# Optimization experiments

Hardware: AMD Instinct MI355X
Metric: run time of the kernel (lower is better)

Reference implementation:

```python
import jax, jax.numpy as jnp
import numpy as np

B, L, T, D, H, DH = 8, 1024, 1024, 768, 12, 64
SPATIAL_DIM = 5


def setup_inputs() -> dict:
    key = jax.random.key(0)
    ks = jax.random.split(key, 12)
    scale = 1.0 / np.sqrt(D)
    inp = {
        "q": jax.random.normal(ks[0], (B, L, D), dtype=jnp.float32),
        "k": jax.random.normal(ks[1], (B, T, D), dtype=jnp.float32),
        "v": jax.random.normal(ks[2], (B, T, D), dtype=jnp.float32),
        "pairwise_locs": jax.random.normal(ks[3], (B, L, T, SPATIAL_DIM), dtype=jnp.float32),
        # last 64 key positions are padding in every batch row (never all-True)
        "key_padding_mask": jnp.broadcast_to(jnp.arange(T) >= T - 64, (B, T)),
        "Wq": jax.random.normal(ks[4], (D, H * DH), dtype=jnp.float32) * scale,
        "bq": jnp.zeros((H * DH,), dtype=jnp.float32),
        "Wk": jax.random.normal(ks[5], (D, H * DH), dtype=jnp.float32) * scale,
        "bk": jnp.zeros((H * DH,), dtype=jnp.float32),
        "Wv": jax.random.normal(ks[6], (D, H * DH), dtype=jnp.float32) * scale,
        "bv": jnp.zeros((H * DH,), dtype=jnp.float32),
        "Wo": jax.random.normal(ks[7], (H * DH, D), dtype=jnp.float32) * scale,
        "bo": jnp.zeros((D,), dtype=jnp.float32),
    }
    return inp


def reference(q, k, v, pairwise_locs, key_padding_mask, Wq, bq, Wk, bk, Wv, bv, Wo, bo):
    # pairwise_locs is accepted but unused in this forward path (as in the source).
    b, l, _ = q.shape
    t = k.shape[1]
    qh = (q @ Wq + bq).reshape(b, l, H, DH)  # b l h d
    kh = (k @ Wk + bk).reshape(b, t, H, DH)  # b t h d
    vh = (v @ Wv + bv).reshape(b, t, H, DH)  # b t h d
    attn = jnp.einsum('blhd,bthd->bhlt', qh, kh) / jnp.sqrt(jnp.float32(DH))
    attn = jnp.where(key_padding_mask[:, None, None, :], -jnp.inf, attn)
    fused_attn = jax.nn.softmax(attn, axis=-1)
    out = jnp.einsum('bhlt,bthd->blhd', fused_attn, vh).reshape(b, l, H * DH)
    return out @ Wo + bo  # dropout is identity in eval mode
```

## Files before the change

### kernel.cpp

```cpp
#include <hip/hip_runtime.h>
#include <hip/hip_bf16.h>
#include <cstdint>
#include <cstddef>
#include <cmath>

#define NB 8
#define NL 1024
#define NT 1024
#define ND 768
#define NH 12
#define NDH 64
#define NM (NB*NL)

typedef short short8 __attribute__((ext_vector_type(8)));
typedef unsigned short ushort4v __attribute__((ext_vector_type(4)));
typedef unsigned int uint4v __attribute__((ext_vector_type(4)));
typedef float f32x4 __attribute__((ext_vector_type(4)));
typedef float float4v __attribute__((ext_vector_type(4)));

__device__ __forceinline__ unsigned short f2bf(float f) {
  union { __hip_bfloat16 h; unsigned short u; } cv;
  cv.h = __float2bfloat16(f);
  return cv.u;
}
__device__ __forceinline__ unsigned pk2(float lo, float hi) {
  return (unsigned)f2bf(lo) | ((unsigned)f2bf(hi) << 16);
}
__device__ __forceinline__ short8 cvt8(float4v x0, float4v x1) {
  union { short8 s; uint4v u; } r;
  r.u = (uint4v){pk2(x0[0], x0[1]), pk2(x0[2], x0[3]),
                 pk2(x1[0], x1[1]), pk2(x1[2], x1[3])};
  return r.s;
}
__device__ __forceinline__ void gll16(const void* g, void* l) {
  __builtin_amdgcn_global_load_lds(
      (const __attribute__((address_space(1))) unsigned int*)g,
      (__attribute__((address_space(3))) unsigned int*)l, 16, 0, 0);
}

__global__ __launch_bounds__(256) void wt_kernel(
    const float* __restrict__ W0, const float* __restrict__ W1,
    const float* __restrict__ W2, const float* __restrict__ W3,
    unsigned short* __restrict__ Wt) {
  __shared__ float tile[32][33];
  const float* W = blockIdx.z == 0 ? W0 : blockIdx.z == 1 ? W1 : blockIdx.z == 2 ? W2 : W3;
  const int k0 = blockIdx.x * 32, n0 = blockIdx.y * 32;
  const int tx = threadIdx.x & 31, ty = threadIdx.x >> 5;
  for (int r = ty; r < 32; r += 8) tile[r][tx] = W[(size_t)(k0 + r) * ND + n0 + tx];
  __syncthreads();
  unsigned short* out = Wt + (size_t)blockIdx.z * ND * ND;
  for (int r = ty; r < 32; r += 8) out[(size_t)(n0 + r) * ND + k0 + tx] = f2bf(tile[tx][r]);
}

template<int MODE>
__global__ __launch_bounds__(256) void gemm_kernel(
    const float* __restrict__ Af0, const float* __restrict__ Af1,
    const unsigned short* __restrict__ Ab, const unsigned short* __restrict__ Wt,
    const float* __restrict__ bias0, const float* __restrict__ bias1,
    unsigned short* __restrict__ outb0, unsigned short* __restrict__ outb1,
    float* __restrict__ outf) {
  constexpr bool AF32 = (MODE != 3);
  __shared__ __align__(16) unsigned char AsRaw[AF32 ? 128 * 64 * 4 : 128 * 64 * 2];
  __shared__ __align__(16) unsigned short Bs[128 * 64];
  const int tid = threadIdx.x, lane = tid & 63, w = tid >> 6;
  const int c = lane & 15, g = lane >> 4;
  const int wrow = w & 1, wcol = w >> 1;
  const int l8 = lane >> 3, l7 = lane & 7, csw = l7 ^ l8;
  const int mbase = blockIdx.x * 128, nbase = blockIdx.y * 128;
  const int z = (MODE == 0) ? blockIdx.z : MODE;

  const float* Af = AF32 ? ((MODE == 0 && z == 1) ? Af1 : Af0) : nullptr;
  const unsigned short* Bt = Wt + (size_t)z * ND * ND;
  const float* bias = (MODE == 0 && z == 1) ? bias1 : bias0;

  f32x4 acc[4][4];
#pragma unroll
  for (int m = 0; m < 4; m++)
#pragma unroll
    for (int n = 0; n < 4; n++) acc[m][n] = (f32x4){0.f, 0.f, 0.f, 0.f};

  for (int k0 = 0; k0 < ND; k0 += 64) {
    if (AF32) {
      float* Asf = (float*)AsRaw;
#pragma unroll
      for (int it = 0; it < 8; it++) {
        int r0 = it * 16 + w * 4;
        int r = r0 + (lane >> 4);
        int gc = (lane & 15) ^ (r & 15);
        gll16(&Af[(size_t)(mbase + r) * ND + k0 + gc * 4], &Asf[r0 * 64]);
      }
    } else {
      unsigned short* Asb = (unsigned short*)AsRaw;
#pragma unroll
      for (int it = 0; it < 4; it++) {
        int r = it * 32 + w * 8 + l8;
        gll16(&Ab[(size_t)(mbase + r) * ND + k0 + csw * 8], &Asb[(it * 32 + w * 8) * 64]);
      }
    }
#pragma unroll
    for (int it = 0; it < 4; it++) {
      int r = it * 32 + w * 8 + l8;
      gll16(&Bt[(size_t)(nbase + r) * ND + k0 + csw * 8], &Bs[(it * 32 + w * 8) * 64]);
    }
    __syncthreads();

#pragma unroll
    for (int ks = 0; ks < 2; ks++) {
      short8 a[4], b[4];
#pragma unroll
      for (int m = 0; m < 4; m++) {
        int r = wrow * 64 + m * 16 + c;
        if (AF32) {
          const float* Asf = (const float*)AsRaw;
          int cc = ks * 8 + g * 2;
          float4v x0 = *(const float4v*)&Asf[r * 64 + ((cc ^ (r & 15)) * 4)];
          float4v x1 = *(const float4v*)&Asf[r * 64 + (((cc + 1) ^ (r & 15)) * 4)];
          a[m] = cvt8(x0, x1);
        } else {
          const unsigned short* Asb = (const unsigned short*)AsRaw;
          a[m] = *(const short8*)&Asb[r * 64 + (((ks * 4 + g) ^ (c & 7)) * 8)];
        }
      }
#pragma unroll
      for (int n = 0; n < 4; n++) {
        int r = wcol * 64 + n * 16 + c;
        b[n] = *(const short8*)&Bs[r * 64 + (((ks * 4 + g) ^ (c & 7)) * 8)];
      }
#pragma unroll
      for (int m = 0; m < 4; m++)
#pragma unroll
        for (int n = 0; n < 4; n++) {
          if (MODE == 2)
            acc[m][n] = __builtin_amdgcn_mfma_f32_16x16x32_bf16(a[m], b[n], acc[m][n], 0, 0, 0);
          else
            acc[m][n] = __builtin_amdgcn_mfma_f32_16x16x32_bf16(b[n], a[m], acc[m][n], 0, 0, 0);
        }
    }
    __syncthreads();
  }

  if (MODE == 2) {
#pragma unroll
    for (int n = 0; n < 4; n++) {
      const int col = nbase + wcol * 64 + n * 16 + c;
      const float bv = bias[col];
      const int h = col >> 6, dd = col & 63;
#pragma unroll
      for (int m = 0; m < 4; m++) {
        const int r0 = mbase + wrow * 64 + m * 16 + g * 4;
        const int bb = r0 >> 10, t = r0 & (NT - 1);
        ushort4v y;
#pragma unroll
        for (int j = 0; j < 4; j++) y[j] = f2bf(acc[m][n][j] + bv);
        *(ushort4v*)&outb0[((size_t)(bb * NH + h) * NDH + dd) * NT + t] = y;
      }
    }
  } else {
    const float scale = (MODE == 0 && z == 0) ? 0.125f * 1.44269504f : 1.0f;
    unsigned short* outb = (MODE == 0) ? (z == 0 ? outb0 : outb1) : nullptr;
#pragma unroll
    for (int n = 0; n < 4; n++) {
      const int colb = nbase + wcol * 64 + n * 16 + g * 4;
      float4v bv4 = *(const float4v*)&bias[colb];
#pragma unroll
      for (int m = 0; m < 4; m++) {
        const int row = mbase + wrow * 64 + m * 16 + c;
        if (MODE == 3) {
          float4v y;
#pragma unroll
          for (int j = 0; j < 4; j++) y[j] = acc[m][n][j] + bv4[j];
          *(float4v*)&outf[(size_t)row * ND + colb] = y;
        } else {
          ushort4v y;
#pragma unroll
          for (int j = 0; j < 4; j++) y[j] = f2bf((acc[m][n][j] + bv4[j]) * scale);
          *(ushort4v*)&outb[(size_t)row * ND + colb] = y;
        }
      }
    }
  }
}

__global__ __launch_bounds__(256) void attn_kernel(
    const unsigned short* __restrict__ qh, const unsigned short* __restrict__ kh,
    const unsigned short* __restrict__ vhT, const unsigned int* __restrict__ mask,
    unsigned short* __restrict__ ao) {
  __shared__ __align__(16) unsigned short Ks[2][64 * 64];
  __shared__ __align__(16) unsigned short Vs[2][64 * 64];
  __shared__ __align__(16) unsigned short Ps[4][32][72];
  const int tid = threadIdx.x, lane = tid & 63, w = tid >> 6;
  const int c = lane & 15, g = lane >> 4;
  const int l8 = lane >> 3, l7 = lane & 7, csw = l7 ^ l8;
  const int qb = blockIdx.x * 128;
  const int b = blockIdx.y / NH, h = blockIdx.y % NH;
  const size_t kbase = (size_t)b * NT * ND + h * NDH;
  const size_t vbase = (size_t)(b * NH + h) * NDH * NT;

  short8 aq[2][2];
#pragma unroll
  for (int half = 0; half < 2; half++) {
    size_t qrow = (size_t)(b * NL + qb + w * 32 + half * 16 + c) * ND + h * NDH;
#pragma unroll
    for (int ks = 0; ks < 2; ks++)
      aq[half][ks] = *(const short8*)&qh[qrow + ks * 32 + g * 8];
  }

  f32x4 o[2][4];
#pragma unroll
  for (int half = 0; half < 2; half++)
#pragma unroll
    for (int f = 0; f < 4; f++) o[half][f] = (f32x4){0.f, 0.f, 0.f, 0.f};
  float mr[2] = {-1e30f, -1e30f}, lr[2] = {0.f, 0.f};

#pragma unroll
  for (int it = 0; it < 2; it++) {
    int r = w * 16 + it * 8 + l8;
    gll16(&kh[kbase + (size_t)r * ND + csw * 8], &Ks[0][(w * 16 + it * 8) * 64]);
    gll16(&vhT[vbase + (size_t)r * NT + csw * 8], &Vs[0][(w * 16 + it * 8) * 64]);
  }
  __syncthreads();

  for (int t0 = 0; t0 < NT; t0 += 64) {
    const int cur = (t0 >> 6) & 1;
    if (t0 + 64 < NT) {
#pragma unroll
      for (int it = 0; it < 2; it++) {
        int r = w * 16 + it * 8 + l8;
        gll16(&kh[kbase + (size_t)(t0 + 64 + r) * ND + csw * 8],
              &Ks[cur ^ 1][(w * 16 + it * 8) * 64]);
        gll16(&vhT[vbase + (size_t)r * NT + (t0 + 64) + csw * 8],
              &Vs[cur ^ 1][(w * 16 + it * 8) * 64]);
      }
    }

    f32x4 s[2][4];
#pragma unroll
    for (int half = 0; half < 2; half++)
#pragma unroll
      for (int n = 0; n < 4; n++) s[half][n] = (f32x4){0.f, 0.f, 0.f, 0.f};
    __builtin_amdgcn_s_setprio(1);
#pragma unroll
    for (int ks = 0; ks < 2; ks++)
#pragma unroll
      for (int n = 0; n < 4; n++) {
        short8 ak = *(const short8*)&Ks[cur][(n * 16 + c) * 64 + (((ks * 4 + g) ^ (c & 7)) * 8)];
        s[0][n] = __builtin_amdgcn_mfma_f32_16x16x32_bf16(ak, aq[0][ks], s[0][n], 0, 0, 0);
        s[1][n] = __builtin_amdgcn_mfma_f32_16x16x32_bf16(ak, aq[1][ks], s[1][n], 0, 0, 0);
      }
    __builtin_amdgcn_s_setprio(0);

    {
      uint4v mm[4];
      unsigned any = 0;
#pragma unroll
      for (int n = 0; n < 4; n++) {
        mm[n] = *(const uint4v*)&mask[(size_t)b * NT + t0 + n * 16 + g * 4];
        any |= mm[n][0] | mm[n][1] | mm[n][2] | mm[n][3];
      }
      if (__any(any != 0u)) {
#pragma unroll
        for (int n = 0; n < 4; n++)
#pragma unroll
          for (int j = 0; j < 4; j++)
            if (mm[n][j]) { s[0][n][j] = -INFINITY; s[1][n][j] = -INFINITY; }
      }
    }

#pragma unroll
    for (int half = 0; half < 2; half++) {
      float m01 = fmaxf(fmaxf(s[half][0][0], s[half][0][1]), fmaxf(s[half][0][2], s[half][0][3]));
      float m23 = fmaxf(fmaxf(s[half][1][0], s[half][1][1]), fmaxf(s[half][1][2], s[half][1][3]));
      float m45 = fmaxf(fmaxf(s[half][2][0], s[half][2][1]), fmaxf(s[half][2][2], s[half][2][3]));
      float m67 = fmaxf(fmaxf(s[half][3][0], s[half][3][1]), fmaxf(s[half][3][2], s[half][3][3]));
      float mt = fmaxf(fmaxf(m01, m23), fmaxf(m45, m67));
      mt = fmaxf(mt, __shfl_xor(mt, 16, 64));
      mt = fmaxf(mt, __shfl_xor(mt, 32, 64));
      if (!__all(mt <= mr[half] + 8.f)) {
        float mnew = fmaxf(mr[half], mt);
        float alpha = exp2f(mr[half] - mnew);
        lr[half] *= alpha;
#pragma unroll
        for (int f = 0; f < 4; f++)
#pragma unroll
          for (int j = 0; j < 4; j++) o[half][f][j] *= alpha;
        mr[half] = mnew;
      }
      float rs = 0.f;
#pragma unroll
      for (int n = 0; n < 4; n++)
#pragma unroll
        for (int j = 0; j < 4; j++) {
          float p = exp2f(s[half][n][j] - mr[half]);
          s[half][n][j] = p;
          rs += p;
        }
      rs += __shfl_xor(rs, 16, 64);
      rs += __shfl_xor(rs, 32, 64);
      lr[half] += rs;
      unsigned* pr = (unsigned*)&Ps[w][half * 16 + c][0];
#pragma unroll
      for (int n = 0; n < 4; n++) {
        pr[n * 8 + g * 2]     = pk2(s[half][n][0], s[half][n][1]);
        pr[n * 8 + g * 2 + 1] = pk2(s[half][n][2], s[half][n][3]);
      }
    }

    __builtin_amdgcn_s_setprio(1);
#pragma unroll
    for (int ks = 0; ks < 2; ks++) {
      short8 bp0 = *(const short8*)&Ps[w][c][ks * 32 + g * 8];
      short8 bp1 = *(const short8*)&Ps[w][16 + c][ks * 32 + g * 8];
#pragma unroll
      for (int f = 0; f < 4; f++) {
        short8 av = *(const short8*)&Vs[cur][(f * 16 + c) * 64 + (((ks * 4 + g) ^ (c & 7)) * 8)];
        o[0][f] = __builtin_amdgcn_mfma_f32_16x16x32_bf16(av, bp0, o[0][f], 0, 0, 0);
        o[1][f] = __builtin_amdgcn_mfma_f32_16x16x32_bf16(av, bp1, o[1][f], 0, 0, 0);
      }
    }
    __builtin_amdgcn_s_setprio(0);
    __syncthreads();
  }

#pragma unroll
  for (int half = 0; half < 2; half++) {
    float inv = 1.f / lr[half];
    size_t row = (size_t)(b * NL + qb + w * 32 + half * 16 + c) * ND + h * NDH;
#pragma unroll
    for (int f = 0; f < 4; f++) {
      ushort4v y;
#pragma unroll
      for (int j = 0; j < 4; j++) y[j] = f2bf(o[half][f][j] * inv);
      *(ushort4v*)&ao[row + f * 16 + g * 4] = y;
    }
  }
}

extern "C" void kernel_launch(void* const* d_in, const int* in_sizes, int n_in,
                              void* d_out, int out_size, void* d_ws, size_t ws_size,
                              hipStream_t stream) {
  const float* q  = (const float*)d_in[0];
  const float* k  = (const float*)d_in[1];
  const float* v  = (const float*)d_in[2];
  const unsigned int* mask = (const unsigned int*)d_in[4];
  const float* Wq = (const float*)d_in[5];
  const float* bq = (const float*)d_in[6];
  const float* Wk = (const float*)d_in[7];
  const float* bk = (const float*)d_in[8];
  const float* Wv = (const float*)d_in[9];
  const float* bv = (const float*)d_in[10];
  const float* Wo = (const float*)d_in[11];
  const float* bo = (const float*)d_in[12];
  float* out = (float*)d_out;

  unsigned short* ws  = (unsigned short*)d_ws;
  unsigned short* Wt  = ws;
  unsigned short* qhb = Wt + (size_t)4 * ND * ND;
  unsigned short* khb = qhb + (size_t)NM * ND;
  unsigned short* vhT = khb + (size_t)NM * ND;
  unsigned short* aob = vhT + (size_t)NM * ND;

  wt_kernel<<<dim3(ND / 32, ND / 32, 4), 256, 0, stream>>>(Wq, Wk, Wv, Wo, Wt);

  gemm_kernel<0><<<dim3(NM / 128, ND / 128, 2), 256, 0, stream>>>(
      q, k, nullptr, Wt, bq, bk, qhb, khb, nullptr);
  gemm_kernel<2><<<dim3(NM / 128, ND / 128), 256, 0, stream>>>(
      v, nullptr, nullptr, Wt, bv, nullptr, vhT, nullptr, nullptr);

  attn_kernel<<<dim3(NL / 128, NB * NH), 256, 0, stream>>>(qhb, khb, vhT, mask, aob);

  gemm_kernel<3><<<dim3(NM / 128, ND / 128), 256, 0, stream>>>(
      nullptr, nullptr, aob, Wt, bo, nullptr, nullptr, nullptr, out);
}
```

Baseline: 172.6 us.

## Skip fully masked key tiles, defer row-sum reduction, convert A to bf16 on load

The attention loop builds a per-tile ballot of the key padding mask and skips all QK, softmax and PV work for tiles that are entirely masked. The per-row sum is kept as a lane-local vector and reduced across lanes only once at the end, and the max-rescale check is merged for both halves so the cross-lane max runs only when rescaling is needed. The fp32 GEMM A-operand is now loaded through registers and converted to bf16 once before being stored to LDS, replacing the async fp32 LDS staging. This halves the LDS footprint and avoids reconverting per k-step, but it gives up the async global-to-LDS copy.

Result: faster. 168.5 us (-2.4%).

```diff
diff --git a/kernel.cpp b/kernel.cpp
--- a/kernel.cpp
+++ b/kernel.cpp
@@ -15,6 +15,7 @@
 typedef short short8 __attribute__((ext_vector_type(8)));
 typedef unsigned short ushort4v __attribute__((ext_vector_type(4)));
 typedef unsigned int uint4v __attribute__((ext_vector_type(4)));
+typedef unsigned int uint2v __attribute__((ext_vector_type(2)));
 typedef float f32x4 __attribute__((ext_vector_type(4)));
 typedef float float4v __attribute__((ext_vector_type(4)));
 
@@ -26,11 +27,11 @@
 __device__ __forceinline__ unsigned pk2(float lo, float hi) {
   return (unsigned)f2bf(lo) | ((unsigned)f2bf(hi) << 16);
 }
-__device__ __forceinline__ short8 cvt8(float4v x0, float4v x1) {
-  union { short8 s; uint4v u; } r;
-  r.u = (uint4v){pk2(x0[0], x0[1]), pk2(x0[2], x0[3]),
-                 pk2(x1[0], x1[1]), pk2(x1[2], x1[3])};
-  return r.s;
+__device__ __forceinline__ f32x4 vmax4(f32x4 a, f32x4 b) {
+  f32x4 r;
+  r[0] = fmaxf(a[0], b[0]); r[1] = fmaxf(a[1], b[1]);
+  r[2] = fmaxf(a[2], b[2]); r[3] = fmaxf(a[3], b[3]);
+  return r;
 }
 __device__ __forceinline__ void gll16(const void* g, void* l) {
   __builtin_amdgcn_global_load_lds(
@@ -59,8 +60,7 @@
     const float* __restrict__ bias0, const float* __restrict__ bias1,
     unsigned short* __restrict__ outb0, unsigned short* __restrict__ outb1,
     float* __restrict__ outf) {
-  constexpr bool AF32 = (MODE != 3);
-  __shared__ __align__(16) unsigned char AsRaw[AF32 ? 128 * 64 * 4 : 128 * 64 * 2];
+  __shared__ __align__(16) unsigned short As[128 * 64];
   __shared__ __align__(16) unsigned short Bs[128 * 64];
   const int tid = threadIdx.x, lane = tid & 63, w = tid >> 6;
   const int c = lane & 15, g = lane >> 4;
@@ -69,7 +69,7 @@
   const int mbase = blockIdx.x * 128, nbase = blockIdx.y * 128;
   const int z = (MODE == 0) ? blockIdx.z : MODE;
 
-  const float* Af = AF32 ? ((MODE == 0 && z == 1) ? Af1 : Af0) : nullptr;
+  const float* Af = (MODE == 0) ? (z == 0 ? Af0 : Af1) : Af0;
   const unsigned short* Bt = Wt + (size_t)z * ND * ND;
   const float* bias = (MODE == 0 && z == 1) ? bias1 : bias0;
 
@@ -80,21 +80,23 @@
     for (int n = 0; n < 4; n++) acc[m][n] = (f32x4){0.f, 0.f, 0.f, 0.f};
 
   for (int k0 = 0; k0 < ND; k0 += 64) {
-    if (AF32) {
-      float* Asf = (float*)AsRaw;
-#pragma unroll
-      for (int it = 0; it < 8; it++) {
-        int r0 = it * 16 + w * 4;
-        int r = r0 + (lane >> 4);
-        int gc = (lane & 15) ^ (r & 15);
-        gll16(&Af[(size_t)(mbase + r) * ND + k0 + gc * 4], &Asf[r0 * 64]);
+    if (MODE != 3) {
+#pragma unroll
+      for (int i = 0; i < 4; i++) {
+        int id = i * 256 + tid;
+        int r = id >> 3, cc = id & 7;
+        const float* src = &Af[(size_t)(mbase + r) * ND + k0 + cc * 8];
+        float4v x0 = *(const float4v*)src;
+        float4v x1 = *(const float4v*)(src + 4);
+        uint4v y = {pk2(x0[0], x0[1]), pk2(x0[2], x0[3]),
+                    pk2(x1[0], x1[1]), pk2(x1[2], x1[3])};
+        *(uint4v*)&As[r * 64 + ((cc ^ (r & 7)) * 8)] = y;
       }
     } else {
-      unsigned short* Asb = (unsigned short*)AsRaw;
 #pragma unroll
       for (int it = 0; it < 4; it++) {
         int r = it * 32 + w * 8 + l8;
-        gll16(&Ab[(size_t)(mbase + r) * ND + k0 + csw * 8], &Asb[(it * 32 + w * 8) * 64]);
+        gll16(&Ab[(size_t)(mbase + r) * ND + k0 + csw * 8], &As[(it * 32 + w * 8) * 64]);
       }
     }
 #pragma unroll
@@ -110,16 +112,7 @@
 #pragma unroll
       for (int m = 0; m < 4; m++) {
         int r = wrow * 64 + m * 16 + c;
-        if (AF32) {
-          const float* Asf = (const float*)AsRaw;
-          int cc = ks * 8 + g * 2;
-          float4v x0 = *(const float4v*)&Asf[r * 64 + ((cc ^ (r & 15)) * 4)];
-          float4v x1 = *(const float4v*)&Asf[r * 64 + (((cc + 1) ^ (r & 15)) * 4)];
-          a[m] = cvt8(x0, x1);
-        } else {
-          const unsigned short* Asb = (const unsigned short*)AsRaw;
-          a[m] = *(const short8*)&Asb[r * 64 + (((ks * 4 + g) ^ (c & 7)) * 8)];
-        }
+        a[m] = *(const short8*)&As[r * 64 + (((ks * 4 + g) ^ (c & 7)) * 8)];
       }
 #pragma unroll
       for (int n = 0; n < 4; n++) {
@@ -205,12 +198,14 @@
       aq[half][ks] = *(const short8*)&qh[qrow + ks * 32 + g * 8];
   }
 
-  f32x4 o[2][4];
-#pragma unroll
-  for (int half = 0; half < 2; half++)
+  f32x4 o[2][4], lrv[2];
+#pragma unroll
+  for (int half = 0; half < 2; half++) {
+    lrv[half] = (f32x4){0.f, 0.f, 0.f, 0.f};
 #pragma unroll
     for (int f = 0; f < 4; f++) o[half][f] = (f32x4){0.f, 0.f, 0.f, 0.f};
-  float mr[2] = {-1e30f, -1e30f}, lr[2] = {0.f, 0.f};
+  }
+  float mr[2] = {-1e30f, -1e30f};
 
 #pragma unroll
   for (int it = 0; it < 2; it++) {
@@ -233,97 +228,98 @@
       }
     }
 
-    f32x4 s[2][4];
-#pragma unroll
-    for (int half = 0; half < 2; half++)
-#pragma unroll
-      for (int n = 0; n < 4; n++) s[half][n] = (f32x4){0.f, 0.f, 0.f, 0.f};
-    __builtin_amdgcn_s_setprio(1);
-#pragma unroll
-    for (int ks = 0; ks < 2; ks++)
-#pragma unroll
-      for (int n = 0; n < 4; n++) {
-        short8 ak = *(const short8*)&Ks[cur][(n * 16 + c) * 64 + (((ks * 4 + g) ^ (c & 7)) * 8)];
-        s[0][n] = __builtin_amdgcn_mfma_f32_16x16x32_bf16(ak, aq[0][ks], s[0][n], 0, 0, 0);
-        s[1][n] = __builtin_amdgcn_mfma_f32_16x16x32_bf16(ak, aq[1][ks], s[1][n], 0, 0, 0);
-      }
-    __builtin_amdgcn_s_setprio(0);
-
-    {
-      uint4v mm[4];
-      unsigned any = 0;
-#pragma unroll
-      for (int n = 0; n < 4; n++) {
-        mm[n] = *(const uint4v*)&mask[(size_t)b * NT + t0 + n * 16 + g * 4];
-        any |= mm[n][0] | mm[n][1] | mm[n][2] | mm[n][3];
-      }
-      if (__any(any != 0u)) {
+    unsigned long long tm = __ballot(mask[(size_t)b * NT + t0 + lane] != 0u);
+
+    if (tm != ~0ull) {
+      f32x4 s[2][4];
+#pragma unroll
+      for (int half = 0; half < 2; half++)
+#pragma unroll
+        for (int n = 0; n < 4; n++) s[half][n] = (f32x4){0.f, 0.f, 0.f, 0.f};
+      __builtin_amdgcn_s_setprio(1);
+#pragma unroll
+      for (int ks = 0; ks < 2; ks++)
+#pragma unroll
+        for (int n = 0; n < 4; n++) {
+          short8 ak = *(const short8*)&Ks[cur][(n * 16 + c) * 64 + (((ks * 4 + g) ^ (c & 7)) * 8)];
+          s[0][n] = __builtin_amdgcn_mfma_f32_16x16x32_bf16(ak, aq[0][ks], s[0][n], 0, 0, 0);
+          s[1][n] = __builtin_amdgcn_mfma_f32_16x16x32_bf16(ak, aq[1][ks], s[1][n], 0, 0, 0);
+        }
+      __builtin_amdgcn_s_setprio(0);
+
+      if (tm) {
+        unsigned long long tms = tm >> (g * 4);
 #pragma unroll
         for (int n = 0; n < 4; n++)
 #pragma unroll
           for (int j = 0; j < 4; j++)
-            if (mm[n][j]) { s[0][n][j] = -INFINITY; s[1][n][j] = -INFINITY; }
-      }
-    }
-
-#pragma unroll
-    for (int half = 0; half < 2; half++) {
-      float m01 = fmaxf(fmaxf(s[half][0][0], s[half][0][1]), fmaxf(s[half][0][2], s[half][0][3]));
-      float m23 = fmaxf(fmaxf(s[half][1][0], s[half][1][1]), fmaxf(s[half][1][2], s[half][1][3]));
-      float m45 = fmaxf(fmaxf(s[half][2][0], s[half][2][1]), fmaxf(s[half][2][2], s[half][2][3]));
-      float m67 = fmaxf(fmaxf(s[half][3][0], s[half][3][1]), fmaxf(s[half][3][2], s[half][3][3]));
-      float mt = fmaxf(fmaxf(m01, m23), fmaxf(m45, m67));
-      mt = fmaxf(mt, __shfl_xor(mt, 16, 64));
-      mt = fmaxf(mt, __shfl_xor(mt, 32, 64));
-      if (!__all(mt <= mr[half] + 8.f)) {
-        float mnew = fmaxf(mr[half], mt);
-        float alpha = exp2f(mr[half] - mnew);
-        lr[half] *= alpha;
-#pragma unroll
-        for (int f = 0; f < 4; f++)
-#pragma unroll
-          for (int j = 0; j < 4; j++) o[half][f][j] *= alpha;
-        mr[half] = mnew;
-      }
-      float rs = 0.f;
-#pragma unroll
-      for (int n = 0; n < 4; n++)
-#pragma unroll
-        for (int j = 0; j < 4; j++) {
-          float p = exp2f(s[half][n][j] - mr[half]);
-          s[half][n][j] = p;
-          rs += p;
-        }
-      rs += __shfl_xor(rs, 16, 64);
-      rs += __shfl_xor(rs, 32, 64);
-      lr[half] += rs;
-      unsigned* pr = (unsigned*)&Ps[w][half * 16 + c][0];
-#pragma unroll
-      for (int n = 0; n < 4; n++) {
-        pr[n * 8 + g * 2]     = pk2(s[half][n][0], s[half][n][1]);
-        pr[n * 8 + g * 2 + 1] = pk2(s[half][n][2], s[half][n][3]);
-      }
-    }
-
-    __builtin_amdgcn_s_setprio(1);
-#pragma unroll
-    for (int ks = 0; ks < 2; ks++) {
-      short8 bp0 = *(const short8*)&Ps[w][c][ks * 32 + g * 8];
-      short8 bp1 = *(const short8*)&Ps[w][16 + c][ks * 32 + g * 8];
-#pragma unroll
-      for (int f = 0; f < 4; f++) {
-        short8 av = *(const short8*)&Vs[cur][(f * 16 + c) * 64 + (((ks * 4 + g) ^ (c & 7)) * 8)];
-        o[0][f] = __builtin_amdgcn_mfma_f32_16x16x32_bf16(av, bp0, o[0][f], 0, 0, 0);
-        o[1][f] = __builtin_amdgcn_mfma_f32_16x16x32_bf16(av, bp1, o[1][f], 0, 0, 0);
-      }
-    }
-    __builtin_amdgcn_s_setprio(0);
+            if ((tms >> (n * 16 + j)) & 1) { s[0][n][j] = -INFINITY; s[1][n][j] = -INFINITY; }
+      }
+
+      float mt[2];
+#pragma unroll
+      for (int half = 0; half < 2; half++) {
+        f32x4 mv = vmax4(vmax4(s[half][0], s[half][1]), vmax4(s[half][2], s[half][3]));
+        mt[half] = fmaxf(fmaxf(mv[0], mv[1]), fmaxf(mv[2], mv[3]));
+      }
+      bool ok = (mt[0] <= mr[0] + 8.f) && (mt[1] <= mr[1] + 8.f);
+      if (!__all(ok)) {
+#pragma unroll
+        for (int half = 0; half < 2; half++) {
+          float mrow = mt[half];
+          mrow = fmaxf(mrow, __shfl_xor(mrow, 16, 64));
+          mrow = fmaxf(mrow, __shfl_xor(mrow, 32, 64));
+          float mnew = fmaxf(mr[half], mrow);
+          float alpha = exp2f(mr[half] - mnew);
+          mr[half] = mnew;
+#pragma unroll
+          for (int j = 0; j < 4; j++) lrv[half][j] *= alpha;
+#pragma unroll
+          for (int f = 0; f < 4; f++)
+#pragma unroll
+            for (int j = 0; j < 4; j++) o[half][f][j] *= alpha;
+        }
+      }
+
+#pragma unroll
+      for (int half = 0; half < 2; half++) {
+#pragma unroll
+        for (int n = 0; n < 4; n++) {
+#pragma unroll
+          for (int j = 0; j < 4; j++) s[half][n][j] = exp2f(s[half][n][j] - mr[half]);
+          lrv[half] += s[half][n];
+        }
+        unsigned* pr = (unsigned*)&Ps[w][half * 16 + c][0];
+#pragma unroll
+        for (int n = 0; n < 4; n++) {
+          uint2v y = {pk2(s[half][n][0], s[half][n][1]), pk2(s[half][n][2], s[half][n][3])};
+          *(uint2v*)&pr[n * 8 + g * 2] = y;
+        }
+      }
+
+      __builtin_amdgcn_s_setprio(1);
+#pragma unroll
+      for (int ks = 0; ks < 2; ks++) {
+        short8 bp0 = *(const short8*)&Ps[w][c][ks * 32 + g * 8];
+        short8 bp1 = *(const short8*)&Ps[w][16 + c][ks * 32 + g * 8];
+#pragma unroll
+        for (int f = 0; f < 4; f++) {
+          short8 av = *(const short8*)&Vs[cur][(f * 16 + c) * 64 + (((ks * 4 + g) ^ (c & 7)) * 8)];
+          o[0][f] = __builtin_amdgcn_mfma_f32_16x16x32_bf16(av, bp0, o[0][f], 0, 0, 0);
+          o[1][f] = __builtin_amdgcn_mfma_f32_16x16x32_bf16(av, bp1, o[1][f], 0, 0, 0);
+        }
+      }
+      __builtin_amdgcn_s_setprio(0);
+    }
     __syncthreads();
   }
 
 #pragma unroll
   for (int half = 0; half < 2; half++) {
-    float inv = 1.f / lr[half];
+    float lr = (lrv[half][0] + lrv[half][1]) + (lrv[half][2] + lrv[half][3]);
+    lr += __shfl_xor(lr, 16, 64);
+    lr += __shfl_xor(lr, 32, 64);
+    float inv = 1.f / lr;
     size_t row = (size_t)(b * NL + qb + w * 32 + half * 16 + c) * ND + h * NDH;
 #pragma unroll
     for (int f = 0; f < 4; f++) {
```
